# Optimization experiments

Hardware: AMD Instinct MI355X
Metric: run time of the kernel (lower is better)

## Reference

```python
import jax, jax.numpy as jnp
import numpy as np

N_NODES = 50000


def gcn_conv(x, src, dst, W, b):
    """PyG GCNConv: y = D^-1/2 (A + I) D^-1/2 (x W) + b, deg counted with self-loops."""
    n = x.shape[0]
    xw = x @ W                                             # [N, out]
    # degree with self-loops (in-degree at dst, +1 for the self-loop)
    deg = jnp.zeros((n,), x.dtype).at[dst].add(1.0) + 1.0  # [N]
    dinv = deg ** -0.5
    coef = dinv[src] * dinv[dst]                           # [E]
    msgs = xw[src] * coef[:, None]                         # [E, out]  (irregular gather)
    agg = jax.ops.segment_sum(msgs, dst, num_segments=n)   # scatter-add
    agg = agg + xw * (dinv * dinv)[:, None]                # self-loop contribution
    return agg + b


def setup_inputs() -> dict:
    key = jax.random.key(0)
    ks = jax.random.split(key, 10)
    d_in, h1, h2, n_cls, e_cls = 64, 256, 128, 2, 2
    x = jax.random.normal(ks[0], (N_NODES, d_in), dtype=jnp.float32)
    edge_index = jax.random.randint(ks[1], (2, 800000), 0, N_NODES, dtype=jnp.int64)

    def glorot(k, shape):
        lim = float(np.sqrt(6.0 / (shape[0] + shape[1])))
        return jax.random.uniform(k, shape, jnp.float32, -lim, lim)

    return {
        "x": x,
        "edge_index": edge_index,
        "W1": glorot(ks[2], (d_in, h1)), "b1": jnp.zeros((h1,), jnp.float32),
        "W2": glorot(ks[3], (h1, h2)), "b2": jnp.zeros((h2,), jnp.float32),
        "node_W": glorot(ks[4], (h2, n_cls)), "node_b": jnp.zeros((n_cls,), jnp.float32),
        "edge_W": glorot(ks[5], (2 * h2, e_cls)), "edge_b": jnp.zeros((e_cls,), jnp.float32),
    }


def reference(x, edge_index, W1, b1, W2, b2, node_W, node_b, edge_W, edge_b):
    src, dst = edge_index[0], edge_index[1]
    h = gcn_conv(x, src, dst, W1, b1)
    h = jax.nn.relu(h)
    embeddings = gcn_conv(h, src, dst, W2, b2)   # last layer: no relu; kept as embeddings
    # dropout is identity in eval mode
    node_x = embeddings @ node_W + node_b        # [N, node_classes]
    edge_feat = jnp.concatenate([embeddings[src], embeddings[dst]], axis=-1)  # [E, 2*h2]
    edge_x = edge_feat @ edge_W + edge_b         # [E, edge_classes]
    return node_x, edge_x
```

## Files before the change

kernel.cpp:

```cpp
#include <hip/hip_runtime.h>

static constexpr int DIN = 64;
static constexpr int H1  = 256;
static constexpr int H2  = 128;

using half8 = _Float16 __attribute__((ext_vector_type(8)));
using f32x4 = float __attribute__((ext_vector_type(4)));

__global__ __launch_bounds__(256) void
k_prep(int* __restrict__ hist, int N,
       const float* __restrict__ x, _Float16* __restrict__ xh, int nvec8,
       const float* __restrict__ W1, _Float16* __restrict__ Wf1,
       const float* __restrict__ W2, const float* __restrict__ nW,
       const float* __restrict__ nb, const float* __restrict__ eW,
       const float* __restrict__ b2, float* __restrict__ Wz8,
       float* __restrict__ consts,
       int NB0, int NB1, int NB2) {
  const int b = blockIdx.x;
  const int t = threadIdx.x;
  if (b < NB0) {
    int i = b * 256 + t;
    if (i < N) hist[i] = 0;
  } else if (b < NB1) {
    int i = (b - NB0) * 256 + t;
    if (i < nvec8) {
      const float4* x4 = (const float4*)x;
      float4 a = x4[i * 2 + 0];
      float4 bb = x4[i * 2 + 1];
      half8 h;
      h[0] = (_Float16)a.x; h[1] = (_Float16)a.y; h[2] = (_Float16)a.z; h[3] = (_Float16)a.w;
      h[4] = (_Float16)bb.x; h[5] = (_Float16)bb.y; h[6] = (_Float16)bb.z; h[7] = (_Float16)bb.w;
      *(half8*)(xh + (size_t)i * 8) = h;
    }
  } else if (b < NB2) {
    int i = (b - NB1) * 256 + t;
    if (i < DIN * H1) {
      int j    = i & 7;
      int lane = (i >> 3) & 63;
      int rest = i >> 9;
      int tt   = rest % (DIN / 32);
      int c    = rest / (DIN / 32);
      int k    = tt * 32 + (lane >> 4) * 8 + j;
      int col  = c * 16 + (lane & 15);
      Wf1[i] = (_Float16)W1[k * H1 + col];
    }
  } else {
    int k = t;
    float acc[6] = {0, 0, 0, 0, 0, 0};
    for (int m = 0; m < H2; ++m) {
      float w = W2[k * H2 + m];
      acc[0] = fmaf(w, nW[m * 2 + 0], acc[0]);
      acc[1] = fmaf(w, nW[m * 2 + 1], acc[1]);
      acc[2] = fmaf(w, eW[m * 2 + 0], acc[2]);
      acc[3] = fmaf(w, eW[m * 2 + 1], acc[3]);
      acc[4] = fmaf(w, eW[(H2 + m) * 2 + 0], acc[4]);
      acc[5] = fmaf(w, eW[(H2 + m) * 2 + 1], acc[5]);
    }
#pragma unroll
    for (int c = 0; c < 6; ++c) Wz8[k * 8 + c] = acc[c];
    Wz8[k * 8 + 6] = 0.0f; Wz8[k * 8 + 7] = 0.0f;
    if (k == 0) {
      float c0 = nb[0], c1 = nb[1], c2 = 0, c3 = 0, c4 = 0, c5 = 0;
      for (int m = 0; m < H2; ++m) {
        float bv = b2[m];
        c0 = fmaf(bv, nW[m * 2 + 0], c0);
        c1 = fmaf(bv, nW[m * 2 + 1], c1);
        c2 = fmaf(bv, eW[m * 2 + 0], c2);
        c3 = fmaf(bv, eW[m * 2 + 1], c3);
        c4 = fmaf(bv, eW[(H2 + m) * 2 + 0], c4);
        c5 = fmaf(bv, eW[(H2 + m) * 2 + 1], c5);
      }
      consts[0] = c0; consts[1] = c1; consts[2] = c2;
      consts[3] = c3; consts[4] = c4; consts[5] = c5;
      consts[6] = 0.0f; consts[7] = 0.0f;
    }
  }
}

__global__ void k_hist(const int* __restrict__ dst, int* __restrict__ hist,
                       unsigned short* __restrict__ rank, int E) {
  int e = blockIdx.x * blockDim.x + threadIdx.x;
  if (e < E) {
    int old = atomicAdd(&hist[dst[e]], 1);
    rank[e] = (unsigned short)old;
  }
}

__global__ void k_scan1(const int* __restrict__ hist, int* __restrict__ offs,
                        int* __restrict__ bsum, float* __restrict__ dinv, int N) {
  __shared__ int ws[4];
  const int t = threadIdx.x;
  const int base = blockIdx.x * 1024 + t * 4;
  int4 v = make_int4(0, 0, 0, 0);
  if (base + 3 < N) v = *(const int4*)(hist + base);
  else {
    if (base + 0 < N) v.x = hist[base + 0];
    if (base + 1 < N) v.y = hist[base + 1];
    if (base + 2 < N) v.z = hist[base + 2];
    if (base + 3 < N) v.w = hist[base + 3];
  }
  if (base + 3 < N) {
    float4 dv = make_float4(rsqrtf((float)v.x + 1.0f), rsqrtf((float)v.y + 1.0f),
                            rsqrtf((float)v.z + 1.0f), rsqrtf((float)v.w + 1.0f));
    *(float4*)(dinv + base) = dv;
  } else {
    if (base + 0 < N) dinv[base + 0] = rsqrtf((float)v.x + 1.0f);
    if (base + 1 < N) dinv[base + 1] = rsqrtf((float)v.y + 1.0f);
    if (base + 2 < N) dinv[base + 2] = rsqrtf((float)v.z + 1.0f);
    if (base + 3 < N) dinv[base + 3] = rsqrtf((float)v.w + 1.0f);
  }
  int tsum = v.x + v.y + v.z + v.w;
  int lane = t & 63, wid = t >> 6;
  int incl = tsum;
#pragma unroll
  for (int off = 1; off < 64; off <<= 1) {
    int u = __shfl_up(incl, off);
    if (lane >= off) incl += u;
  }
  if (lane == 63) ws[wid] = incl;
  __syncthreads();
  int wbase = 0;
  for (int w = 0; w < wid; ++w) wbase += ws[w];
  int excl = wbase + incl - tsum;
  int4 o;
  o.x = excl;
  o.y = excl + v.x;
  o.z = excl + v.x + v.y;
  o.w = excl + v.x + v.y + v.z;
  if (base + 3 < N) *(int4*)(offs + base) = o;
  else {
    if (base + 0 < N) offs[base + 0] = o.x;
    if (base + 1 < N) offs[base + 1] = o.y;
    if (base + 2 < N) offs[base + 2] = o.z;
    if (base + 3 < N) offs[base + 3] = o.w;
  }
  if (t == 255) bsum[blockIdx.x] = wbase + incl;
}

__global__ void k_scan3(int* __restrict__ offs, const int* __restrict__ bsum,
                        int nb, int N, int E) {
  __shared__ int sbase;
  const int t = threadIdx.x;
  if (t < 64) {
    int v = (t < nb) ? bsum[t] : 0;
    int incl = v;
#pragma unroll
    for (int off = 1; off < 64; off <<= 1) {
      int u = __shfl_up(incl, off);
      if (t >= off) incl += u;
    }
    if (t == (int)blockIdx.x) sbase = incl - v;
  }
  __syncthreads();
  int b = sbase;
  if (blockIdx.x == 0 && t == 0) offs[N] = E;
  if (b == 0) return;
  int base = blockIdx.x * 1024 + t * 4;
  if (base + 3 < N) {
    int4 v = *(int4*)(offs + base);
    v.x += b; v.y += b; v.z += b; v.w += b;
    *(int4*)(offs + base) = v;
  } else {
    for (int k = 0; k < 4; ++k) if (base + k < N) offs[base + k] += b;
  }
}

__global__ void k_build(const int* __restrict__ src, const int* __restrict__ dst,
                        const unsigned short* __restrict__ rank,
                        const int* __restrict__ offs,
                        unsigned short* __restrict__ csr, int E) {
  int e = blockIdx.x * blockDim.x + threadIdx.x;
  if (e < E) {
    int d = dst[e];
    int pos = offs[d] + (int)rank[e];
    __builtin_nontemporal_store((unsigned short)src[e], &csr[pos]);
  }
}

template<int C, bool BIAS>
__global__ __launch_bounds__(256) void
k_gather(const int* __restrict__ offs, const unsigned short* __restrict__ csr,
         const float* __restrict__ dinv, const _Float16* __restrict__ xw,
         const float* __restrict__ bias, _Float16* __restrict__ out, int N) {
  constexpr int GSIZE = C / 8;
  constexpr int NE    = 64 / GSIZE;
  int wave = (int)((blockIdx.x * (size_t)blockDim.x + threadIdx.x) >> 6);
  int lane = threadIdx.x & 63;
  if (wave >= N) return;
  int group = lane / GSIZE;
  int sub   = lane % GSIZE;
  int ch0   = sub * 8;
  float dv = dinv[wave];
  int j0 = offs[wave], j1 = offs[wave + 1];

  float acc[8];
  if (group == 0) {
    half8 v = *(const half8*)(xw + (size_t)wave * C + ch0);
    float sc = dv * dv;
#pragma unroll
    for (int k = 0; k < 8; ++k) acc[k] = (float)v[k] * sc;
  } else {
#pragma unroll
    for (int k = 0; k < 8; ++k) acc[k] = 0.0f;
  }

  for (int base = j0; base < j1; base += 64) {
    int myj = base + lane;
    int s_l = 0; float dv_l = 0.0f;
    if (myj < j1) { s_l = (int)csr[myj]; dv_l = dinv[s_l]; }
    int cnt = min(64, j1 - base);
    for (int k = 0; k < cnt; k += NE) {
      int idx = k + group;
      int   s = __shfl(s_l, idx);
      float c = __shfl(dv_l, idx) * dv;
      if (c != 0.0f) {
        half8 v = *(const half8*)(xw + (size_t)s * C + ch0);
#pragma unroll
        for (int k2 = 0; k2 < 8; ++k2) acc[k2] = fmaf((float)v[k2], c, acc[k2]);
      }
    }
  }

#pragma unroll
  for (int off = GSIZE; off < 64; off <<= 1) {
#pragma unroll
    for (int k = 0; k < 8; ++k) acc[k] += __shfl_xor(acc[k], off);
  }

  if (group == 0) {
    half8 o;
#pragma unroll
    for (int k = 0; k < 8; ++k) {
      float v = acc[k] + (BIAS ? bias[ch0 + k] : 0.0f);
      o[k] = (_Float16)v;
    }
    *(half8*)(out + (size_t)wave * C + ch0) = o;
  }
}

__global__ __launch_bounds__(256) void
k_mgemm_z(const _Float16* __restrict__ A, const _Float16* __restrict__ Wf,
          const float* __restrict__ bias, const float* __restrict__ Wz8,
          float* __restrict__ z, int M) {
  constexpr int K = DIN, NOUT = H1;
  constexpr int NC = NOUT / 16;
  constexpr int NT = K / 32;
  const int wave = threadIdx.x >> 6;
  const int lane = threadIdx.x & 63;
  const int rowbase = blockIdx.x * 128 + wave * 32;
  if (rowbase >= M) return;
  const int r  = lane & 15;
  const int kb = lane >> 4;
  int row0 = rowbase + r;       if (row0 >= M) row0 = M - 1;
  int row1 = rowbase + 16 + r;  if (row1 >= M) row1 = M - 1;
  const _Float16* a0p = A + (size_t)row0 * K + kb * 8;
  const _Float16* a1p = A + (size_t)row1 * K + kb * 8;

  f32x4 acc[2][NC];
#pragma unroll
  for (int rb = 0; rb < 2; ++rb)
#pragma unroll
    for (int c = 0; c < NC; ++c) acc[rb][c] = (f32x4)0.0f;

#pragma unroll
  for (int t = 0; t < NT; ++t) {
    half8 a0 = *(const half8*)(a0p + t * 32);
    half8 a1 = *(const half8*)(a1p + t * 32);
#pragma unroll
    for (int c = 0; c < NC; ++c) {
      half8 bf = ((const half8*)Wf)[(size_t)(c * NT + t) * 64 + lane];
      acc[0][c] = __builtin_amdgcn_mfma_f32_16x16x32_f16(a0, bf, acc[0][c], 0, 0, 0);
      acc[1][c] = __builtin_amdgcn_mfma_f32_16x16x32_f16(a1, bf, acc[1][c], 0, 0, 0);
    }
  }

  float zc[2][4][6];
#pragma unroll
  for (int rb = 0; rb < 2; ++rb)
#pragma unroll
    for (int j = 0; j < 4; ++j)
#pragma unroll
      for (int ch = 0; ch < 6; ++ch) zc[rb][j][ch] = 0.0f;

#pragma unroll
  for (int c = 0; c < NC; ++c) {
    int col = c * 16 + r;
    const float* wp = Wz8 + col * 8;
    float4 w0 = *(const float4*)wp;
    float2 w1 = *(const float2*)(wp + 4);
    float bv = bias[col];
#pragma unroll
    for (int rb = 0; rb < 2; ++rb) {
#pragma unroll
      for (int j = 0; j < 4; ++j) {
        float hv = fmaxf(acc[rb][c][j] + bv, 0.0f);
        zc[rb][j][0] = fmaf(hv, w0.x, zc[rb][j][0]);
        zc[rb][j][1] = fmaf(hv, w0.y, zc[rb][j][1]);
        zc[rb][j][2] = fmaf(hv, w0.z, zc[rb][j][2]);
        zc[rb][j][3] = fmaf(hv, w0.w, zc[rb][j][3]);
        zc[rb][j][4] = fmaf(hv, w1.x, zc[rb][j][4]);
        zc[rb][j][5] = fmaf(hv, w1.y, zc[rb][j][5]);
      }
    }
  }

#pragma unroll
  for (int off = 1; off < 16; off <<= 1) {
#pragma unroll
    for (int rb = 0; rb < 2; ++rb)
#pragma unroll
      for (int j = 0; j < 4; ++j)
#pragma unroll
        for (int ch = 0; ch < 6; ++ch)
          zc[rb][j][ch] += __shfl_xor(zc[rb][j][ch], off);
  }

  if (r == 0) {
#pragma unroll
    for (int rb = 0; rb < 2; ++rb) {
      int growbase = rowbase + rb * 16 + kb * 4;
#pragma unroll
      for (int j = 0; j < 4; ++j) {
        int grow = growbase + j;
        if (grow < M) {
          float4 lo = make_float4(zc[rb][j][0], zc[rb][j][1], zc[rb][j][2], zc[rb][j][3]);
          float4 hi = make_float4(zc[rb][j][4], zc[rb][j][5], 0.0f, 0.0f);
          *(float4*)(z + (size_t)grow * 8)     = lo;
          *(float4*)(z + (size_t)grow * 8 + 4) = hi;
        }
      }
    }
  }
}

__global__ __launch_bounds__(256) void
k_gatherz(const int* __restrict__ offs, const unsigned short* __restrict__ csr,
          const float* __restrict__ dinv, const float* __restrict__ z,
          const float* __restrict__ consts,
          float* __restrict__ node_out, float* __restrict__ p, float* __restrict__ q,
          int N) {
  int wave = (int)((blockIdx.x * (size_t)blockDim.x + threadIdx.x) >> 6);
  int lane = threadIdx.x & 63;
  int half = lane >> 5;
  int node = wave * 2 + half;
  if (node >= N) return;
  int lane32 = lane & 31;
  int group  = lane32 >> 1;
  int sub    = lane32 & 1;
  int hb     = half << 5;
  float dv = dinv[node];
  int j0 = offs[node], j1 = offs[node + 1];

  float4 acc = make_float4(0.0f, 0.0f, 0.0f, 0.0f);
  if (group == 0) {
    float4 v = *(const float4*)(z + (size_t)node * 8 + sub * 4);
    float sc = dv * dv;
    acc = make_float4(v.x * sc, v.y * sc, v.z * sc, v.w * sc);
  }

  for (int base = j0; base < j1; base += 32) {
    int myj = base + lane32;
    int s_l = 0; float dv_l = 0.0f;
    if (myj < j1) { s_l = (int)csr[myj]; dv_l = dinv[s_l]; }
    int cnt = min(32, j1 - base);
    for (int k = 0; k < cnt; k += 16) {
      int idx = k + group;
      int   s = __shfl(s_l, hb + idx);
      float c = __shfl(dv_l, hb + idx) * dv;
      if (c != 0.0f) {
        float4 v = *(const float4*)(z + (size_t)s * 8 + sub * 4);
        acc.x = fmaf(v.x, c, acc.x);
        acc.y = fmaf(v.y, c, acc.y);
        acc.z = fmaf(v.z, c, acc.z);
        acc.w = fmaf(v.w, c, acc.w);
      }
    }
  }

#pragma unroll
  for (int off = 2; off < 32; off <<= 1) {
    acc.x += __shfl_xor(acc.x, off);
    acc.y += __shfl_xor(acc.y, off);
    acc.z += __shfl_xor(acc.z, off);
    acc.w += __shfl_xor(acc.w, off);
  }

  if (lane32 == 0) {
    float2 no = make_float2(acc.x + consts[0], acc.y + consts[1]);
    float2 pp = make_float2(acc.z + consts[2], acc.w + consts[3]);
    *(float2*)(node_out + (size_t)node * 2) = no;
    *(float2*)(p + (size_t)node * 2) = pp;
  } else if (lane32 == 1) {
    float2 qq = make_float2(acc.x + consts[4], acc.y + consts[5]);
    *(float2*)(q + (size_t)node * 2) = qq;
  }
}

__global__ void k_edge(const int* __restrict__ src, const int* __restrict__ dst,
                       const float* __restrict__ p, const float* __restrict__ q,
                       const float* __restrict__ eb, float* __restrict__ eout, int E) {
  int i = blockIdx.x * blockDim.x + threadIdx.x;
  int e = i * 2;
  float e0 = eb[0], e1 = eb[1];
  if (e + 1 < E) {
    int2 s2 = *(const int2*)(src + e);
    int2 d2 = *(const int2*)(dst + e);
    float2 P0 = *(const float2*)(p + (size_t)s2.x * 2);
    float2 Q0 = *(const float2*)(q + (size_t)d2.x * 2);
    float2 P1 = *(const float2*)(p + (size_t)s2.y * 2);
    float2 Q1 = *(const float2*)(q + (size_t)d2.y * 2);
    float4 o;
    o.x = P0.x + Q0.x + e0;
    o.y = P0.y + Q0.y + e1;
    o.z = P1.x + Q1.x + e0;
    o.w = P1.y + Q1.y + e1;
    *(float4*)(eout + (size_t)e * 2) = o;
  } else if (e < E) {
    int s = src[e], d = dst[e];
    float2 P = *(const float2*)(p + (size_t)s * 2);
    float2 Q = *(const float2*)(q + (size_t)d * 2);
    float2 o;
    o.x = P.x + Q.x + e0;
    o.y = P.y + Q.y + e1;
    *(float2*)(eout + (size_t)e * 2) = o;
  }
}

extern "C" void kernel_launch(void* const* d_in, const int* in_sizes, int n_in,
                              void* d_out, int out_size, void* d_ws, size_t ws_size,
                              hipStream_t stream) {
  const float* x   = (const float*)d_in[0];
  const int*   ei  = (const int*)d_in[1];
  const float* W1  = (const float*)d_in[2];
  const float* b1  = (const float*)d_in[3];
  const float* W2  = (const float*)d_in[4];
  const float* b2  = (const float*)d_in[5];
  const float* nW  = (const float*)d_in[6];
  const float* nb  = (const float*)d_in[7];
  const float* eW  = (const float*)d_in[8];
  const float* eb  = (const float*)d_in[9];

  const int N = in_sizes[0] / DIN;
  const int E = in_sizes[1] / 2;
  const int* src = ei;
  const int* dst = ei + E;

  float* fws   = (float*)d_ws;
  float* dinv  = fws;
  float* p     = dinv + N;
  float* q     = p + 2 * (size_t)N;
  float* z     = q + 2 * (size_t)N;
  float* Wz8   = z + 8 * (size_t)N;
  float* consts = Wz8 + 2048;
  _Float16* xh    = (_Float16*)(consts + 8);
  _Float16* aggxh = xh + (size_t)DIN * N;
  _Float16* Wf1   = aggxh + (size_t)DIN * N;
  int* hist = (int*)(Wf1 + DIN * H1);
  int* offs = hist + N;
  int* bsum = offs + N + 1;
  unsigned short* rank = (unsigned short*)(bsum + 64);
  unsigned short* csr  = rank + E;

  float* node_out = (float*)d_out;
  float* edge_out = (float*)d_out + 2 * (size_t)N;

  const int nb_blk = (N + 1023) / 1024;
  const int nvec8  = N * DIN / 8;

  const int NB0 = (N + 255) / 256;
  const int NB1 = NB0 + (nvec8 + 255) / 256;
  const int NB2 = NB1 + (DIN * H1 + 255) / 256;
  const int NBP = NB2 + 1;

  k_prep<<<NBP, 256, 0, stream>>>(hist, N, x, xh, nvec8, W1, Wf1,
                                  W2, nW, nb, eW, b2, Wz8, consts, NB0, NB1, NB2);
  k_hist<<<(E + 255) / 256, 256, 0, stream>>>(dst, hist, rank, E);
  k_scan1<<<nb_blk, 256, 0, stream>>>(hist, offs, bsum, dinv, N);
  k_scan3<<<nb_blk, 256, 0, stream>>>(offs, bsum, nb_blk, N, E);
  k_build<<<(E + 255) / 256, 256, 0, stream>>>(src, dst, rank, offs, csr, E);

  k_gather<DIN, false><<<(N + 3) / 4, 256, 0, stream>>>(offs, csr, dinv, xh, nullptr, aggxh, N);
  k_mgemm_z<<<(N + 127) / 128, 256, 0, stream>>>(aggxh, Wf1, b1, Wz8, z, N);

  k_gatherz<<<((N + 1) / 2 + 3) / 4, 256, 0, stream>>>(offs, csr, dinv, z, consts, node_out, p, q, N);

  k_edge<<<((E + 1) / 2 + 255) / 256, 256, 0, stream>>>(src, dst, p, q, eb, edge_out, E);
}
```

Baseline: 148.3 us.

## Pack source index and fp16 dinv into CSR entries; pair-process edges; 4 nodes per wave

CSR entries become 32-bit words holding the source node index in the high 16 bits and the source's fp16 inverse-sqrt degree in the low bits. This removes the dependent dinv[src] gather inside both aggregation kernels. The hist and build kernels now handle two edges per thread with vectorized loads. k_gatherz maps four nodes per wave instead of two to fit the average degree better. In exchange the normalization coefficient loses precision by being stored in fp16, the CSR doubles in size, and node indices must fit in 16 bits.

```diff
diff --git a/kernel.cpp b/kernel.cpp
--- a/kernel.cpp
+++ b/kernel.cpp
@@ -6,6 +6,19 @@
 
 using half8 = _Float16 __attribute__((ext_vector_type(8)));
 using f32x4 = float __attribute__((ext_vector_type(4)));
+
+__device__ __forceinline__ unsigned short f2h_bits(float f) {
+  _Float16 h = (_Float16)f;
+  unsigned short u;
+  __builtin_memcpy(&u, &h, 2);
+  return u;
+}
+__device__ __forceinline__ float h_bits2f(unsigned u) {
+  unsigned short us = (unsigned short)(u & 0xffffu);
+  _Float16 h;
+  __builtin_memcpy(&h, &us, 2);
+  return (float)h;
+}
 
 __global__ __launch_bounds__(256) void
 k_prep(int* __restrict__ hist, int N,
@@ -79,10 +92,17 @@
 
 __global__ void k_hist(const int* __restrict__ dst, int* __restrict__ hist,
                        unsigned short* __restrict__ rank, int E) {
-  int e = blockIdx.x * blockDim.x + threadIdx.x;
-  if (e < E) {
-    int old = atomicAdd(&hist[dst[e]], 1);
-    rank[e] = (unsigned short)old;
+  int i = blockIdx.x * blockDim.x + threadIdx.x;
+  int e = i * 2;
+  if (e + 1 < E) {
+    int2 d2 = *(const int2*)(dst + e);
+    int r0 = atomicAdd(&hist[d2.x], 1);
+    int r1 = atomicAdd(&hist[d2.y], 1);
+    unsigned pk = (unsigned)(r0 & 0xffff) | ((unsigned)(r1 & 0xffff) << 16);
+    *(unsigned*)(rank + e) = pk;
+  } else if (e < E) {
+    int r = atomicAdd(&hist[dst[e]], 1);
+    rank[e] = (unsigned short)r;
   }
 }
 
@@ -167,23 +187,33 @@
 
 __global__ void k_build(const int* __restrict__ src, const int* __restrict__ dst,
                         const unsigned short* __restrict__ rank,
-                        const int* __restrict__ offs,
-                        unsigned short* __restrict__ csr, int E) {
-  int e = blockIdx.x * blockDim.x + threadIdx.x;
-  if (e < E) {
-    int d = dst[e];
+                        const int* __restrict__ offs, const float* __restrict__ dinv,
+                        unsigned* __restrict__ csr, int E) {
+  int i = blockIdx.x * blockDim.x + threadIdx.x;
+  int e = i * 2;
+  if (e + 1 < E) {
+    int2 s2 = *(const int2*)(src + e);
+    int2 d2 = *(const int2*)(dst + e);
+    unsigned rr = *(const unsigned*)(rank + e);
+    int pos0 = offs[d2.x] + (int)(rr & 0xffffu);
+    int pos1 = offs[d2.y] + (int)(rr >> 16);
+    unsigned v0 = ((unsigned)s2.x << 16) | f2h_bits(dinv[s2.x]);
+    unsigned v1 = ((unsigned)s2.y << 16) | f2h_bits(dinv[s2.y]);
+    __builtin_nontemporal_store(v0, &csr[pos0]);
+    __builtin_nontemporal_store(v1, &csr[pos1]);
+  } else if (e < E) {
+    int s = src[e], d = dst[e];
     int pos = offs[d] + (int)rank[e];
-    __builtin_nontemporal_store((unsigned short)src[e], &csr[pos]);
-  }
-}
-
-template<int C, bool BIAS>
+    unsigned v = ((unsigned)s << 16) | f2h_bits(dinv[s]);
+    __builtin_nontemporal_store(v, &csr[pos]);
+  }
+}
+
 __global__ __launch_bounds__(256) void
-k_gather(const int* __restrict__ offs, const unsigned short* __restrict__ csr,
-         const float* __restrict__ dinv, const _Float16* __restrict__ xw,
-         const float* __restrict__ bias, _Float16* __restrict__ out, int N) {
-  constexpr int GSIZE = C / 8;
-  constexpr int NE    = 64 / GSIZE;
+k_gather64(const int* __restrict__ offs, const unsigned* __restrict__ csr,
+           const float* __restrict__ dinv, const _Float16* __restrict__ xw,
+           _Float16* __restrict__ out, int N) {
+  constexpr int C = 64, GSIZE = 8, NE = 8;
   int wave = (int)((blockIdx.x * (size_t)blockDim.x + threadIdx.x) >> 6);
   int lane = threadIdx.x & 63;
   if (wave >= N) return;
@@ -206,14 +236,14 @@
 
   for (int base = j0; base < j1; base += 64) {
     int myj = base + lane;
-    int s_l = 0; float dv_l = 0.0f;
-    if (myj < j1) { s_l = (int)csr[myj]; dv_l = dinv[s_l]; }
+    unsigned u_l = 0;
+    if (myj < j1) u_l = csr[myj];
     int cnt = min(64, j1 - base);
     for (int k = 0; k < cnt; k += NE) {
-      int idx = k + group;
-      int   s = __shfl(s_l, idx);
-      float c = __shfl(dv_l, idx) * dv;
-      if (c != 0.0f) {
+      unsigned u = (unsigned)__shfl((int)u_l, k + group);
+      if (u != 0) {
+        int   s = (int)(u >> 16);
+        float c = h_bits2f(u) * dv;
         half8 v = *(const half8*)(xw + (size_t)s * C + ch0);
 #pragma unroll
         for (int k2 = 0; k2 < 8; ++k2) acc[k2] = fmaf((float)v[k2], c, acc[k2]);
@@ -230,10 +260,7 @@
   if (group == 0) {
     half8 o;
 #pragma unroll
-    for (int k = 0; k < 8; ++k) {
-      float v = acc[k] + (BIAS ? bias[ch0 + k] : 0.0f);
-      o[k] = (_Float16)v;
-    }
+    for (int k = 0; k < 8; ++k) o[k] = (_Float16)acc[k];
     *(half8*)(out + (size_t)wave * C + ch0) = o;
   }
 }
@@ -334,20 +361,20 @@
 }
 
 __global__ __launch_bounds__(256) void
-k_gatherz(const int* __restrict__ offs, const unsigned short* __restrict__ csr,
+k_gatherz(const int* __restrict__ offs, const unsigned* __restrict__ csr,
           const float* __restrict__ dinv, const float* __restrict__ z,
           const float* __restrict__ consts,
           float* __restrict__ node_out, float* __restrict__ p, float* __restrict__ q,
           int N) {
   int wave = (int)((blockIdx.x * (size_t)blockDim.x + threadIdx.x) >> 6);
   int lane = threadIdx.x & 63;
-  int half = lane >> 5;
-  int node = wave * 2 + half;
+  int quad = lane >> 4;
+  int node = wave * 4 + quad;
   if (node >= N) return;
-  int lane32 = lane & 31;
-  int group  = lane32 >> 1;
-  int sub    = lane32 & 1;
-  int hb     = half << 5;
+  int l16   = lane & 15;
+  int group = l16 >> 1;
+  int sub   = l16 & 1;
+  int hb    = quad << 4;
   float dv = dinv[node];
   int j0 = offs[node], j1 = offs[node + 1];
 
@@ -358,16 +385,16 @@
     acc = make_float4(v.x * sc, v.y * sc, v.z * sc, v.w * sc);
   }
 
-  for (int base = j0; base < j1; base += 32) {
-    int myj = base + lane32;
-    int s_l = 0; float dv_l = 0.0f;
-    if (myj < j1) { s_l = (int)csr[myj]; dv_l = dinv[s_l]; }
-    int cnt = min(32, j1 - base);
-    for (int k = 0; k < cnt; k += 16) {
-      int idx = k + group;
-      int   s = __shfl(s_l, hb + idx);
-      float c = __shfl(dv_l, hb + idx) * dv;
-      if (c != 0.0f) {
+  for (int base = j0; base < j1; base += 16) {
+    int myj = base + l16;
+    unsigned u_l = 0;
+    if (myj < j1) u_l = csr[myj];
+    int cnt = min(16, j1 - base);
+    for (int k = 0; k < cnt; k += 8) {
+      unsigned u = (unsigned)__shfl((int)u_l, hb + k + group);
+      if (u != 0) {
+        int   s = (int)(u >> 16);
+        float c = h_bits2f(u) * dv;
         float4 v = *(const float4*)(z + (size_t)s * 8 + sub * 4);
         acc.x = fmaf(v.x, c, acc.x);
         acc.y = fmaf(v.y, c, acc.y);
@@ -378,19 +405,19 @@
   }
 
 #pragma unroll
-  for (int off = 2; off < 32; off <<= 1) {
+  for (int off = 2; off < 16; off <<= 1) {
     acc.x += __shfl_xor(acc.x, off);
     acc.y += __shfl_xor(acc.y, off);
     acc.z += __shfl_xor(acc.z, off);
     acc.w += __shfl_xor(acc.w, off);
   }
 
-  if (lane32 == 0) {
+  if (l16 == 0) {
     float2 no = make_float2(acc.x + consts[0], acc.y + consts[1]);
     float2 pp = make_float2(acc.z + consts[2], acc.w + consts[3]);
     *(float2*)(node_out + (size_t)node * 2) = no;
     *(float2*)(p + (size_t)node * 2) = pp;
-  } else if (lane32 == 1) {
+  } else if (l16 == 1) {
     float2 qq = make_float2(acc.x + consts[4], acc.y + consts[5]);
     *(float2*)(q + (size_t)node * 2) = qq;
   }
@@ -459,7 +486,7 @@
   int* offs = hist + N;
   int* bsum = offs + N + 1;
   unsigned short* rank = (unsigned short*)(bsum + 64);
-  unsigned short* csr  = rank + E;
+  unsigned* csr = (unsigned*)(rank + E);
 
   float* node_out = (float*)d_out;
   float* edge_out = (float*)d_out + 2 * (size_t)N;
@@ -474,15 +501,18 @@
 
   k_prep<<<NBP, 256, 0, stream>>>(hist, N, x, xh, nvec8, W1, Wf1,
                                   W2, nW, nb, eW, b2, Wz8, consts, NB0, NB1, NB2);
-  k_hist<<<(E + 255) / 256, 256, 0, stream>>>(dst, hist, rank, E);
+  k_hist<<<((E + 1) / 2 + 255) / 256, 256, 0, stream>>>(dst, hist, rank, E);
   k_scan1<<<nb_blk, 256, 0, stream>>>(hist, offs, bsum, dinv, N);
   k_scan3<<<nb_blk, 256, 0, stream>>>(offs, bsum, nb_blk, N, E);
-  k_build<<<(E + 255) / 256, 256, 0, stream>>>(src, dst, rank, offs, csr, E);
-
-  k_gather<DIN, false><<<(N + 3) / 4, 256, 0, stream>>>(offs, csr, dinv, xh, nullptr, aggxh, N);
+  k_build<<<((E + 1) / 2 + 255) / 256, 256, 0, stream>>>(src, dst, rank, offs, dinv, csr, E);
+
+  k_gather64<<<(N + 3) / 4, 256, 0, stream>>>(offs, csr, dinv, xh, aggxh, N);
   k_mgemm_z<<<(N + 127) / 128, 256, 0, stream>>>(aggxh, Wf1, b1, Wz8, z, N);
 
-  k_gatherz<<<((N + 1) / 2 + 3) / 4, 256, 0, stream>>>(offs, csr, dinv, z, consts, node_out, p, q, N);
+  {
+    int waves = (N + 3) / 4;
+    k_gatherz<<<(waves + 3) / 4, 256, 0, stream>>>(offs, csr, dinv, z, consts, node_out, p, q, N);
+  }
 
   k_edge<<<((E + 1) / 2 + 255) / 256, 256, 0, stream>>>(src, dst, p, q, eb, edge_out, E);
 }
```

New measurement: 144.4 us. 2.6% less time.
